# Optimization experiments

Hardware: AMD Instinct MI355X
Metric: run time of the kernel (lower is better)

Reference implementation:

```python
import jax, jax.numpy as jnp
import numpy as np

H = 4       # num_heads
K = 16      # neighbors
EPS = 1e-5  # BatchNorm eps (eval mode with running stats)


def _bn1d(y, g, b, m, v):
    # y: [B, C, N]; per-channel affine batchnorm (eval mode)
    return (y - m[:, None]) * (g[:, None] / jnp.sqrt(v[:, None] + EPS)) + b[:, None]


def setup_inputs() -> dict:
    key = jax.random.key(0)
    ks = jax.random.split(key, 10)
    B, C, N = 2, 256, 4096
    s = 0.02
    inp = {
        'x': jax.random.normal(ks[0], (B, C, N), jnp.float32),
        'xyz': jax.random.normal(ks[1], (B, 3, N), jnp.float32),
        'Wq': jax.random.normal(ks[2], (C, C), jnp.float32) * s,
        'Wkv': jax.random.normal(ks[3], (2 * C, C), jnp.float32) * s,
        'Wproj': jax.random.normal(ks[4], (C, C), jnp.float32) * s,
        'rp_w1': jax.random.normal(ks[5], (C, 3), jnp.float32) * s,
        'rp_g': jnp.ones((C,), jnp.float32),
        'rp_b': jnp.zeros((C,), jnp.float32),
        'rp_m': jnp.zeros((C,), jnp.float32),
        'rp_v': jnp.ones((C,), jnp.float32),
        'rp_w2': jax.random.normal(ks[6], (C, C), jnp.float32) * s,
        'bn1_g': jnp.ones((C,), jnp.float32), 'bn1_b': jnp.zeros((C,), jnp.float32),
        'bn1_m': jnp.zeros((C,), jnp.float32), 'bn1_v': jnp.ones((C,), jnp.float32),
        'bn2_g': jnp.ones((C,), jnp.float32), 'bn2_b': jnp.zeros((C,), jnp.float32),
        'bn2_m': jnp.zeros((C,), jnp.float32), 'bn2_v': jnp.ones((C,), jnp.float32),
        'ffn_w1': jax.random.normal(ks[7], (4 * C, C), jnp.float32) * s,
        'ffn_b1': jnp.zeros((4 * C,), jnp.float32),
        'ffn_w2': jax.random.normal(ks[8], (C, 4 * C), jnp.float32) * s,
        'ffn_b2': jnp.zeros((C,), jnp.float32),
    }
    return inp


def reference(x, xyz, Wq, Wkv, Wproj, rp_w1, rp_g, rp_b, rp_m, rp_v, rp_w2,
              bn1_g, bn1_b, bn1_m, bn1_v, bn2_g, bn2_b, bn2_m, bn2_v,
              ffn_w1, ffn_b1, ffn_w2, ffn_b2):
    B, C, N = x.shape
    d = C // H
    scale = d ** -0.5

    # --- KNN indices ---
    pts = xyz.transpose(0, 2, 1)                       # [B,N,3]
    sq = jnp.sum(pts * pts, -1)                        # [B,N]
    dists = sq[:, :, None] + sq[:, None, :] - 2.0 * jnp.einsum('bnc,bmc->bnm', pts, pts)
    idx = jax.lax.top_k(-dists, K)[1]                  # [B,N,K]

    # --- q, k, v (1x1 conv == matmul over channels) ---
    q = jnp.einsum('oc,bcn->bon', Wq, x).reshape(B, H, d, N)
    kv = jnp.einsum('oc,bcn->bon', Wkv, x)
    kf = kv[:, :C].transpose(0, 2, 1)                  # [B,N,C]
    vf = kv[:, C:].transpose(0, 2, 1)                  # [B,N,C]

    gather = jax.vmap(lambda f, i: f[i])               # per-batch KNN gather
    kg = gather(kf, idx).reshape(B, N, K, H, d)
    vg = gather(vf, idx).reshape(B, N, K, H, d)

    # --- attention logits: per-neighbor dot ---
    logits = jnp.einsum('bhdn,bnkhd->bhnk', q, kg) * scale

    # --- relative-position bias (1x1 conv MLP over rel coords) ---
    nbr = gather(pts, idx)                             # [B,N,K,3]
    rel = nbr - pts[:, :, None, :]                     # [B,N,K,3]
    h1 = jnp.einsum('oc,bnkc->bnko', rp_w1, rel)
    h1 = (h1 - rp_m) * (rp_g / jnp.sqrt(rp_v + EPS)) + rp_b
    h1 = jax.nn.relu(h1)
    h2 = jnp.einsum('oc,bnkc->bnko', rp_w2, h1).reshape(B, N, K, H, d)
    logits = logits + jnp.einsum('bnkhd->bhnk', h2)    # sum over d

    attn = jax.nn.softmax(logits, axis=-1)             # [B,H,N,K]
    out = jnp.einsum('bhnk,bnkhd->bhdn', attn, vg).reshape(B, C, N)
    out = jnp.einsum('oc,bcn->bon', Wproj, out)

    x1 = _bn1d(x + out, bn1_g, bn1_b, bn1_m, bn1_v)
    h = jax.nn.relu(jnp.einsum('oc,bcn->bon', ffn_w1, x1) + ffn_b1[:, None])
    f = jnp.einsum('oc,bcn->bon', ffn_w2, h) + ffn_b2[:, None]
    return _bn1d(x1 + f, bn2_g, bn2_b, bn2_m, bn2_v)
```

## Files before the change

### kernel.cpp

```cpp
#include <hip/hip_runtime.h>
#include <math.h>

#define BB   2
#define CC   256
#define NPT  4096
#define HH   4
#define DD   64
#define KNN  16
#define EPSBN 1e-5f

typedef __attribute__((ext_vector_type(8))) short short8;
typedef __attribute__((ext_vector_type(4))) float f32x4;

typedef __attribute__((address_space(3))) unsigned int lds_u32;
typedef const __attribute__((address_space(1))) unsigned int glb_u32;
__device__ __forceinline__ void gl_lds16(const void* g, void* l) {
  __builtin_amdgcn_global_load_lds((glb_u32*)g, (lds_u32*)l, 16, 0, 0);
}

__device__ __forceinline__ unsigned short f2b(float f) {
  union { float f; unsigned int u; } v; v.f = f;
  unsigned int r = (v.u + 0x7FFFu + ((v.u >> 16) & 1u)) >> 16;
  return (unsigned short)r;
}
__device__ __forceinline__ void up2(unsigned int u, float& a, float& b) {
  union { unsigned int x; float f; } lo, hi;
  lo.x = u << 16; hi.x = u & 0xffff0000u;
  a = lo.f; b = hi.f;
}
__device__ __forceinline__ void up16(uint4 u0, uint4 u1, float* f) {
  up2(u0.x, f[0], f[1]);  up2(u0.y, f[2], f[3]);
  up2(u0.z, f[4], f[5]);  up2(u0.w, f[6], f[7]);
  up2(u1.x, f[8], f[9]);  up2(u1.y, f[10], f[11]);
  up2(u1.z, f[12], f[13]); up2(u1.w, f[14], f[15]);
}

__device__ __forceinline__ unsigned int med3u(unsigned int a, unsigned int b, unsigned int c) {
  unsigned int d;
  asm("v_med3_u32 %0, %1, %2, %3" : "=v"(d) : "v"(a), "v"(b), "v"(c));
  return d;
}

__device__ __forceinline__
void wcast_body(const float* Wq, const float* Wkv, const float* Wp,
                const float* W1, const float* W2,
                unsigned short* oQKV, unsigned short* oP,
                unsigned short* o1, unsigned short* o2,
                const float* rp_w1, const float* rp_g, const float* rp_b,
                const float* rp_m, const float* rp_v, const float* rp_w2,
                float4* w1f, float4* W2t, int blk) {
  if (blk == 3072) {
    int c = threadIdx.x;
    float s  = rp_g[c] / sqrtf(rp_v[c] + EPSBN);
    float b0 = rp_b[c] - rp_m[c] * s;
    w1f[c] = make_float4(rp_w1[c*3+0]*s, rp_w1[c*3+1]*s, rp_w1[c*3+2]*s, b0);
    float a0=0.f,a1=0.f,a2=0.f,a3=0.f;
    for (int o = 0; o < 64; o++) {
      a0 += rp_w2[(      o)*CC + c];
      a1 += rp_w2[( 64 + o)*CC + c];
      a2 += rp_w2[(128 + o)*CC + c];
      a3 += rp_w2[(192 + o)*CC + c];
    }
    W2t[c] = make_float4(a0,a1,a2,a3);
    return;
  }
  int i = blk * 256 + threadIdx.x;
  if (i < 65536)        oQKV[i] = f2b(Wq[i]);
  else if (i < 196608)  oQKV[i] = f2b(Wkv[i - 65536]);
  else if (i < 262144)  oP[i - 196608] = f2b(Wp[i - 196608]);
  else if (i < 524288)  o1[i - 262144] = f2b(W1[i - 262144]);
  else                  o2[i - 524288] = f2b(W2[i - 524288]);
}

__device__ __forceinline__
void xcast_body(const float* x, unsigned short* xb, float* xf,
                float (*T)[65], int bx, int by, int bz) {
  int n0 = bx * 64, c0 = by * 64, bb = bz;
  int tid = threadIdx.x;
  {
    int crow = tid >> 2, ns = (tid & 3) * 16;
    const float* xp = x + ((size_t)(bb*CC + c0 + crow))*NPT + n0 + ns;
#pragma unroll
    for (int i = 0; i < 4; i++) {
      float4 v = ((const float4*)xp)[i];
      T[crow][ns + i*4 + 0] = v.x; T[crow][ns + i*4 + 1] = v.y;
      T[crow][ns + i*4 + 2] = v.z; T[crow][ns + i*4 + 3] = v.w;
    }
  }
  __syncthreads();
  {
    int nrow = tid >> 2, cs = (tid & 3) * 16;
    float vals[16];
#pragma unroll
    for (int i = 0; i < 16; i++) vals[i] = T[cs + i][nrow];
    size_t orow = ((size_t)(bb*NPT + n0 + nrow))*CC + c0 + cs;
#pragma unroll
    for (int i = 0; i < 4; i++)
      *(float4*)&xf[orow + i*4] = make_float4(vals[i*4], vals[i*4+1], vals[i*4+2], vals[i*4+3]);
    unsigned short us[16];
#pragma unroll
    for (int i = 0; i < 16; i++) us[i] = f2b(vals[i]);
    *(uint4*)&xb[orow]     = *(const uint4*)&us[0];
    *(uint4*)&xb[orow + 8] = *(const uint4*)&us[8];
  }
}

#define MPROC(M4, MI) { \
    float nd = fmaf(qx2, (M4).x, fmaf(qy2, (M4).y, fmaf(qz2, (M4).z, (M4).w + qsq))); \
    nd = fmaxf(nd, 0.f); \
    unsigned int key = (__float_as_uint(nd) & 0xFFFFFE00u) | (unsigned int)(MI); \
    k15 = med3u(key, k14, k15); k14 = med3u(key, k13, k14); \
    k13 = med3u(key, k12, k13); k12 = med3u(key, k11, k12); \
    k11 = med3u(key, k10, k11); k10 = med3u(key, k9,  k10); \
    k9  = med3u(key, k8,  k9 ); k8  = med3u(key, k7,  k8 ); \
    k7  = med3u(key, k6,  k7 ); k6  = med3u(key, k5,  k6 ); \
    k5  = med3u(key, k4,  k5 ); k4  = med3u(key, k3,  k4 ); \
    k3  = med3u(key, k2,  k3 ); k2  = med3u(key, k1,  k2 ); \
    k1  = med3u(key, k0,  k1 ); k0  = min(key, k0); }

__device__ __forceinline__
void knn_partial_body(const float* xyz, unsigned int* Pp, float4* sp,
                      int s, int qg, int b) {
  const float* base = xyz + (size_t)b * 3 * NPT;
  int c0 = s * 512;
  for (int i = threadIdx.x; i < 512; i += 256) {
    float mx = base[c0 + i], my = base[NPT + c0 + i], mz = base[2*NPT + c0 + i];
    sp[i] = make_float4(mx, my, mz, mx*mx + my*my + mz*mz);
  }
  int lane = threadIdx.x & 63;
  int wv   = threadIdx.x >> 6;
  int qn   = qg * 64 + lane;
  float qx = base[qn], qy = base[NPT + qn], qz = base[2*NPT + qn];
  float qsq = qx*qx + qy*qy + qz*qz;
  float qx2 = -2.f*qx, qy2 = -2.f*qy, qz2 = -2.f*qz;
  __syncthreads();

  unsigned int k0=0xFFFFFFFFu,k1=0xFFFFFFFFu,k2=0xFFFFFFFFu,k3=0xFFFFFFFFu,
               k4=0xFFFFFFFFu,k5=0xFFFFFFFFu,k6=0xFFFFFFFFu,k7=0xFFFFFFFFu,
               k8=0xFFFFFFFFu,k9=0xFFFFFFFFu,k10=0xFFFFFFFFu,k11=0xFFFFFFFFu,
               k12=0xFFFFFFFFu,k13=0xFFFFFFFFu,k14=0xFFFFFFFFu,k15=0xFFFFFFFFu;

  int sb = wv * 128;
  for (int mm = 0; mm < 128; mm += 4) {
    float4 a = sp[sb+mm], bq = sp[sb+mm+1], cq = sp[sb+mm+2], dq = sp[sb+mm+3];
    MPROC(a,  sb+mm)
    MPROC(bq, sb+mm+1)
    MPROC(cq, sb+mm+2)
    MPROC(dq, sb+mm+3)
  }

  int gq = b * NPT + qn;
  uint4* out = (uint4*)(Pp + (size_t)gq * 512 + (size_t)(s*4 + wv) * 16);
  out[0] = make_uint4(k0,  k1,  k2,  k3);
  out[1] = make_uint4(k4,  k5,  k6,  k7);
  out[2] = make_uint4(k8,  k9,  k10, k11);
  out[3] = make_uint4(k12, k13, k14, k15);
}

__global__ __launch_bounds__(256) __attribute__((amdgpu_waves_per_eu(1, 4)))
void stage1_kernel(const float* x, unsigned short* xb, float* xf,
                   const float* xyz, unsigned int* Pp,
                   const float* Wq, const float* Wkv, const float* Wp,
                   const float* W1, const float* W2,
                   unsigned short* oQKV, unsigned short* oP,
                   unsigned short* o1, unsigned short* o2,
                   const float* rp_w1, const float* rp_g, const float* rp_b,
                   const float* rp_m, const float* rp_v, const float* rp_w2,
                   float4* w1f, float4* W2t) {
  __shared__ __align__(16) char smem[64*65*4];
  int bi = blockIdx.x;
  if (bi < 1024) {
    knn_partial_body(xyz, Pp, (float4*)smem, bi & 7, (bi >> 3) & 63, bi >> 9);
  } else if (bi < 1536) {
    int i = bi - 1024;
    xcast_body(x, xb, xf, (float(*)[65])smem, i & 63, (i >> 6) & 3, i >> 8);
  } else {
    wcast_body(Wq, Wkv, Wp, W1, W2, oQKV, oP, o1, o2,
               rp_w1, rp_g, rp_b, rp_m, rp_v, rp_w2, w1f, W2t, bi - 1536);
  }
}

__device__ __forceinline__ unsigned long long min64(unsigned long long a, unsigned long long b) {
  return a < b ? a : b;
}
__device__ __forceinline__ void ce64(unsigned long long& x, unsigned long long& y) {
  unsigned long long a = x, b = y;
  bool lt = a < b;
  x = lt ? a : b;
  y = lt ? b : a;
}
__device__ __forceinline__
void knn_merge_body(const unsigned int* Pp, int* idx_out, int blk) {
  int wv   = threadIdx.x >> 6;
  int lane = threadIdx.x & 63;
  int gq   = blk * 4 + wv;
  const uint4* base = (const uint4*)(Pp + (size_t)gq * 512);
  uint4 v0 = base[lane*2], v1 = base[lane*2 + 1];
  unsigned int gb = (unsigned int)(lane >> 3) * 512u;
  unsigned long long a[16];
  {
    unsigned int ks[8] = {v0.x, v0.y, v0.z, v0.w, v1.x, v1.y, v1.z, v1.w};
#pragma unroll
    for (int t = 0; t < 8; t++)
      a[t] = ((unsigned long long)(ks[t] & 0xFFFFFE00u) << 32) | (gb + (ks[t] & 0x1FFu));
#pragma unroll
    for (int t = 8; t < 16; t++) a[t] = ~0ull;
  }
#pragma unroll
  for (int r = 0; r < 6; r++) {
    const int m = 1 << r;
    unsigned long long t[16];
#pragma unroll
    for (int i = 0; i < 16; i++) {
      unsigned long long pb = __shfl_xor(a[15 - i], m, 64);
      t[i] = min64(a[i], pb);
    }
    if (r < 5) {
#pragma unroll
      for (int d = 8; d >= 1; d >>= 1)
#pragma unroll
        for (int i = 0; i < 16; i++)
          if ((i & d) == 0) ce64(t[i], t[i + d]);
    }
#pragma unroll
    for (int i = 0; i < 16; i++) a[i] = t[i];
  }
  if (lane == 0) {
    int4* o = (int4*)(idx_out + gq*16);
    o[0] = make_int4((int)(unsigned)a[0],  (int)(unsigned)a[1],
                     (int)(unsigned)a[2],  (int)(unsigned)a[3]);
    o[1] = make_int4((int)(unsigned)a[4],  (int)(unsigned)a[5],
                     (int)(unsigned)a[6],  (int)(unsigned)a[7]);
    o[2] = make_int4((int)(unsigned)a[8],  (int)(unsigned)a[9],
                     (int)(unsigned)a[10], (int)(unsigned)a[11]);
    o[3] = make_int4((int)(unsigned)a[12], (int)(unsigned)a[13],
                     (int)(unsigned)a[14], (int)(unsigned)a[15]);
  }
}

struct MG {
  const unsigned short* A; const unsigned short* Wt; int K; int M;
  unsigned short* OutB; float* OutF;
  const float* bias; const float* resid;
  const float* bng; const float* bnb; const float* bnm; const float* bnv;
};

template<int EPI, int NT>
__device__ __forceinline__ void mgemm_body(const MG& p, int bx, int by, int bz) {
  __shared__ unsigned short As[NT*64*64];
  __shared__ unsigned short Bs[64*64];
  const int tid  = threadIdx.x;
  const int bb   = bz;
  const int n0   = bx * (NT*64);
  const int m0   = by * 64;
  const int lane = tid & 63;
  const int wv   = tid >> 6;
  const int l15  = lane & 15;
  const int quad = lane >> 4;
  const int K    = p.K;
  const int WR   = NT*16;

  f32x4 acc[NT][4];
#pragma unroll
  for (int i = 0; i < NT; i++)
#pragma unroll
    for (int j = 0; j < 4; j++) acc[i][j] = (f32x4){0.f, 0.f, 0.f, 0.f};

  const int srow = wv*8 + (lane >> 3);
  const int pseg = lane & 7;
  const unsigned short* Abase = p.A  + (size_t)bb*NPT*K;

  for (int c0 = 0; c0 < K; c0 += 64) {
#pragma unroll
    for (int t = 0; t < NT*2; t++) {
      int row = t*32 + srow;
      int ls  = pseg ^ (row & 7);
      gl_lds16(Abase + (size_t)(n0 + row)*K + c0 + ls*8,
               &As[wv*512 + t*2048 + lane*8]);
    }
#pragma unroll
    for (int t = 0; t < 2; t++) {
      int row = t*32 + srow;
      int ls  = pseg ^ (row & 7);
      gl_lds16(p.Wt + (size_t)(m0 + row)*K + c0 + ls*8,
               &Bs[wv*512 + t*2048 + lane*8]);
    }
    __syncthreads();
    short8 bf[4][2];
#pragma unroll
    for (int mt = 0; mt < 4; mt++)
#pragma unroll
      for (int kk = 0; kk < 2; kk++) {
        int row = mt*16 + l15;
        int ps  = (kk*4 + quad) ^ (row & 7);
        bf[mt][kk] = *(const short8*)&Bs[row*64 + ps*8];
      }
#pragma unroll
    for (int nt = 0; nt < NT; nt++)
#pragma unroll
      for (int kk = 0; kk < 2; kk++) {
        int row = wv*WR + nt*16 + l15;
        int ps  = (kk*4 + quad) ^ (row & 7);
        short8 af = *(const short8*)&As[row*64 + ps*8];
#pragma unroll
        for (int mt = 0; mt < 4; mt++)
          acc[nt][mt] = __builtin_amdgcn_mfma_f32_16x16x32_bf16(af, bf[mt][kk], acc[nt][mt], 0, 0, 0);
      }
    __syncthreads();
  }

  if (EPI == 0 || EPI == 1) {
    float bs[4];
#pragma unroll
    for (int mt = 0; mt < 4; mt++)
      bs[mt] = (EPI == 1) ? p.bias[m0 + mt*16 + l15] : 0.f;
#pragma unroll
    for (int nt = 0; nt < NT; nt++)
#pragma unroll
      for (int reg = 0; reg < 4; reg++) {
        size_t row = ((size_t)(bb*NPT + n0 + wv*WR + nt*16 + quad*4 + reg))*p.M + m0;
#pragma unroll
        for (int mt = 0; mt < 4; mt++) {
          float v = acc[nt][mt][reg] + bs[mt];
          if (EPI == 1) v = fmaxf(v, 0.f);
          p.OutB[row + mt*16 + l15] = f2b(v);
        }
      }
  } else if (EPI == 2) {
    float sc[4], sh[4];
#pragma unroll
    for (int mt = 0; mt < 4; mt++) {
      int m = m0 + mt*16 + l15;
      float s = p.bng[m] / sqrtf(p.bnv[m] + EPSBN);
      sc[mt] = s; sh[mt] = p.bnb[m] - p.bnm[m]*s;
    }
#pragma unroll
    for (int nt = 0; nt < NT; nt++)
#pragma unroll
      for (int reg = 0; reg < 4; reg++) {
        size_t row = ((size_t)(bb*NPT + n0 + wv*WR + nt*16 + quad*4 + reg))*p.M + m0;
#pragma unroll
        for (int mt = 0; mt < 4; mt++) {
          float r = p.resid[row + mt*16 + l15];
          float v = (acc[nt][mt][reg] + r)*sc[mt] + sh[mt];
          p.OutF[row + mt*16 + l15] = v;
          p.OutB[row + mt*16 + l15] = f2b(v);
        }
      }
  } else {
    __shared__ float Tb[4][4][16*17];
    float sc[4], sh[4], bs[4];
#pragma unroll
    for (int mt = 0; mt < 4; mt++) {
      int m = m0 + mt*16 + l15;
      float s = p.bng[m] / sqrtf(p.bnv[m] + EPSBN);
      sc[mt] = s; sh[mt] = p.bnb[m] - p.bnm[m]*s;
      bs[mt] = p.bias[m];
    }
#pragma unroll
    for (int nt = 0; nt < NT; nt++) {
#pragma unroll
      for (int reg = 0; reg < 4; reg++) {
        size_t row = ((size_t)(bb*NPT + n0 + wv*WR + nt*16 + quad*4 + reg))*p.M + m0;
#pragma unroll
        for (int mt = 0; mt < 4; mt++) {
          float r = p.resid[row + mt*16 + l15];
          float v = (acc[nt][mt][reg] + bs[mt] + r)*sc[mt] + sh[mt];
          Tb[wv][mt][(quad*4 + reg)*17 + l15] = v;
        }
      }
      __syncthreads();
#pragma unroll
      for (int mt = 0; mt < 4; mt++)
#pragma unroll
        for (int reg = 0; reg < 4; reg++) {
          float v = Tb[wv][mt][l15*17 + quad*4 + reg];
          p.OutF[((size_t)(bb*p.M + m0 + mt*16 + quad*4 + reg))*NPT
                 + n0 + wv*WR + nt*16 + l15] = v;
        }
      __syncthreads();
    }
  }
}

template<int EPI, int NT>
__global__ __launch_bounds__(256)
void mgemm_kernel(MG p) { mgemm_body<EPI, NT>(p, blockIdx.x, blockIdx.y, blockIdx.z); }

__global__ __launch_bounds__(256)
void stage2_kernel(const unsigned int* Pp, int* idx, MG pqkv) {
  int bi = blockIdx.x;
  if (bi < 2048) {
    knn_merge_body(Pp, idx, bi);
  } else {
    int i = bi - 2048;
    mgemm_body<0, 2>(pqkv, i & 31, (i >> 5) % 12, i / 384);
  }
}

__global__ __launch_bounds__(256, 4)
void attn_kernel(const unsigned short* __restrict__ qkv, const float4* __restrict__ w1f,
                 const float4* __restrict__ W2t, const float* __restrict__ xyz,
                 const int* __restrict__ idx, unsigned short* __restrict__ attn_b) {
  __shared__ float4 sw1[256];
  __shared__ float4 sw2[256];
  __shared__ int   sidx[4][16];
  __shared__ float srel[4][16][4];
  __shared__ float sbias[4][16][4];
  __shared__ float red[4][16*68];
  int tid = threadIdx.x;
  int bn0 = blockIdx.x * 4;
  int b   = bn0 >> 12;
  sw1[tid] = w1f[tid];
  sw2[tid] = W2t[tid];
  if (tid < 64) {
    int p = tid >> 4, kk = tid & 15;
    int bn = bn0 + p, n = bn & 4095;
    int j = idx[bn*16 + kk];
    sidx[p][kk] = j;
    const float* pb = xyz + (size_t)b * 3 * NPT;
    srel[p][kk][0] = pb[j]         - pb[n];
    srel[p][kk][1] = pb[NPT + j]   - pb[NPT + n];
    srel[p][kk][2] = pb[2*NPT + j] - pb[2*NPT + n];
  }
  __syncthreads();
  {
    int kk = tid >> 4, cs = tid & 15;
    float rx[4], ry[4], rz[4], h[4][4];
#pragma unroll
    for (int p = 0; p < 4; p++) {
      rx[p] = srel[p][kk][0]; ry[p] = srel[p][kk][1]; rz[p] = srel[p][kk][2];
#pragma unroll
      for (int q = 0; q < 4; q++) h[p][q] = 0.f;
    }
#pragma unroll
    for (int i = 0; i < 16; i++) {
      int c = cs*16 + ((i + cs) & 15);
      float4 w  = sw1[c];
      float4 w2 = sw2[c];
#pragma unroll
      for (int p = 0; p < 4; p++) {
        float t0 = fmaxf(fmaf(rx[p], w.x, fmaf(ry[p], w.y, fmaf(rz[p], w.z, w.w))), 0.f);
        h[p][0] = fmaf(t0, w2.x, h[p][0]); h[p][1] = fmaf(t0, w2.y, h[p][1]);
        h[p][2] = fmaf(t0, w2.z, h[p][2]); h[p][3] = fmaf(t0, w2.w, h[p][3]);
      }
    }
#pragma unroll
    for (int off = 1; off < 16; off <<= 1)
#pragma unroll
      for (int p = 0; p < 4; p++)
#pragma unroll
        for (int q = 0; q < 4; q++)
          h[p][q] += __shfl_xor(h[p][q], off, 64);
    if (cs == 0)
#pragma unroll
      for (int p = 0; p < 4; p++)
#pragma unroll
        for (int q = 0; q < 4; q++) sbias[p][kk][q] = h[p][q];
  }
  __syncthreads();
  int wv   = tid >> 6;
  int lane = tid & 63;
  int k    = lane >> 2;
  int c4   = lane & 3;
  int ch0  = wv*64 + c4*16;
  size_t base = (size_t)(b*NPT) * 768;
#pragma unroll 1
  for (int p = 0; p < 4; p++) {
    int bn = bn0 + p;
    size_t rowq = (size_t)bn * 768;
    float qf[16];
    {
      uint4 q0 = *(const uint4*)(qkv + rowq + ch0);
      uint4 q1 = *(const uint4*)(qkv + rowq + ch0 + 8);
      up16(q0, q1, qf);
    }
    int j = sidx[p][k];
    float dot = 0.f;
    {
      const unsigned short* krow = qkv + base + (size_t)j*768 + 256 + ch0;
      uint4 k0 = *(const uint4*)(krow);
      uint4 k1 = *(const uint4*)(krow + 8);
      float kf[16];
      up16(k0, k1, kf);
#pragma unroll
      for (int i = 0; i < 16; i++) dot = fmaf(qf[i], kf[i], dot);
    }
    dot += __shfl_xor(dot, 1, 64);
    dot += __shfl_xor(dot, 2, 64);
    float logit = dot * 0.125f + sbias[p][k][wv];
    float mx = logit;
#pragma unroll
    for (int off = 4; off < 64; off <<= 1) mx = fmaxf(mx, __shfl_xor(mx, off, 64));
    float e = __expf(logit - mx);
    float ssum = e;
#pragma unroll
    for (int off = 4; off < 64; off <<= 1) ssum += __shfl_xor(ssum, off, 64);
    float w = e / ssum;
    {
      const unsigned short* vrow = qkv + base + (size_t)j*768 + 512 + ch0;
      uint4 v0 = *(const uint4*)(vrow);
      uint4 v1 = *(const uint4*)(vrow + 8);
      float vf[16];
      up16(v0, v1, vf);
      float* dst = &red[wv][k*68 + c4*16];
#pragma unroll
      for (int g = 0; g < 4; g++)
        ((float4*)dst)[g] = make_float4(w*vf[g*4], w*vf[g*4+1], w*vf[g*4+2], w*vf[g*4+3]);
    }
    __syncthreads();
    float o = 0.f;
#pragma unroll
    for (int kk2 = 0; kk2 < 16; kk2++) o += red[wv][kk2*68 + lane];
    attn_b[(size_t)bn*256 + wv*64 + lane] = f2b(o);
    __syncthreads();
  }
}

extern "C" void kernel_launch(void* const* d_in, const int* in_sizes, int n_in,
                              void* d_out, int out_size, void* d_ws, size_t ws_size,
                              hipStream_t stream) {
  const float* x     = (const float*)d_in[0];
  const float* xyz   = (const float*)d_in[1];
  const float* Wq    = (const float*)d_in[2];
  const float* Wkv   = (const float*)d_in[3];
  const float* Wproj = (const float*)d_in[4];
  const float* rp_w1 = (const float*)d_in[5];
  const float* rp_g  = (const float*)d_in[6];
  const float* rp_b  = (const float*)d_in[7];
  const float* rp_m  = (const float*)d_in[8];
  const float* rp_v  = (const float*)d_in[9];
  const float* rp_w2 = (const float*)d_in[10];
  const float* bn1_g = (const float*)d_in[11];
  const float* bn1_b = (const float*)d_in[12];
  const float* bn1_m = (const float*)d_in[13];
  const float* bn1_v = (const float*)d_in[14];
  const float* bn2_g = (const float*)d_in[15];
  const float* bn2_b = (const float*)d_in[16];
  const float* bn2_m = (const float*)d_in[17];
  const float* bn2_v = (const float*)d_in[18];
  const float* ffn_w1 = (const float*)d_in[19];
  const float* ffn_b1 = (const float*)d_in[20];
  const float* ffn_w2 = (const float*)d_in[21];
  const float* ffn_b2 = (const float*)d_in[22];

  char* ws = (char*)d_ws;
  float4* w1f = (float4*)(ws + 0);
  float4* W2t = (float4*)(ws + 4096);
  int*    idx = (int*)  (ws + 8192);
  const size_t oA = 532480;
  unsigned int*   Pp     = (unsigned int*)(ws + oA);
  unsigned short* attn_b = (unsigned short*)(ws + oA);
  float*          x1f    = (float*)(ws + oA + (4u<<20));
  unsigned short* x1b    = (unsigned short*)(ws + oA + (12u<<20));
  unsigned short* h_b    = (unsigned short*)(ws + oA + (16u<<20));
  const size_t oB = oA + (32u<<20);
  unsigned short* Wqkv_b  = (unsigned short*)(ws + oB);
  unsigned short* Wproj_b = (unsigned short*)(ws + oB + 393216);
  unsigned short* W1_b    = (unsigned short*)(ws + oB + 524288);
  unsigned short* W2_b    = (unsigned short*)(ws + oB + 1048576);
  unsigned short* xb      = (unsigned short*)(ws + oB + 1572864);
  float*          xf      = (float*)(ws + oB + 1572864 + (4u<<20));
  unsigned short* qkv     = (unsigned short*)(ws + oB + 1572864 + (12u<<20));

  stage1_kernel<<<4609, 256, 0, stream>>>(x, xb, xf, xyz, Pp,
                                          Wq, Wkv, Wproj, ffn_w1, ffn_w2,
                                          Wqkv_b, Wproj_b, W1_b, W2_b,
                                          rp_w1, rp_g, rp_b, rp_m, rp_v, rp_w2,
                                          w1f, W2t);

  MG pqkv = {xb, Wqkv_b, 256, 768, qkv, nullptr,
             nullptr, nullptr, nullptr, nullptr, nullptr, nullptr};
  stage2_kernel<<<2816, 256, 0, stream>>>(Pp, idx, pqkv);

  attn_kernel<<<(BB*NPT)/4, 256, 0, stream>>>(qkv, w1f, W2t, xyz, idx, attn_b);

  MG pproj = {attn_b, Wproj_b, 256, 256, x1b, x1f,
              nullptr, xf, bn1_g, bn1_b, bn1_m, bn1_v};
  mgemm_kernel<2, 1><<<dim3(64, 4, BB), 256, 0, stream>>>(pproj);

  MG pf1 = {x1b, W1_b, 256, 1024, h_b, nullptr,
            ffn_b1, nullptr, nullptr, nullptr, nullptr, nullptr};
  mgemm_kernel<1, 2><<<dim3(32, 16, BB), 256, 0, stream>>>(pf1);

  MG pf2 = {h_b, W2_b, 1024, 256, nullptr, (float*)d_out,
            ffn_b2, x1f, bn2_g, bn2_b, bn2_m, bn2_v};
  mgemm_kernel<3, 1><<<dim3(64, 4, BB), 256, 0, stream>>>(pf2);
}
```

Measured before the change: 222.1 us.

## Merge KNN partial top-16 lists within block via LDS before global write

Each KNN partial block now merges its four per-wave top-16 lists through shared memory with bitonic merges, so only one list per 512-candidate chunk is written. The partial buffer shrinks fourfold, and the merge stage reads 8 lists per query with one query per 8 lanes, running 3 shuffle rounds instead of 6 on a much smaller grid. The GEMM blocks are scheduled first in stage2. This adds LDS traffic and barriers to the partial kernel and enlarges its shared memory, which may lower occupancy.

```diff
diff --git a/kernel.cpp b/kernel.cpp
--- a/kernel.cpp
+++ b/kernel.cpp
@@ -39,6 +39,10 @@
   unsigned int d;
   asm("v_med3_u32 %0, %1, %2, %3" : "=v"(d) : "v"(a), "v"(b), "v"(c));
   return d;
+}
+__device__ __forceinline__ void ce32(unsigned int& x, unsigned int& y) {
+  unsigned int a = min(x, y), b = max(x, y);
+  x = a; y = b;
 }
 
 __device__ __forceinline__
@@ -119,8 +123,9 @@
     k1  = med3u(key, k0,  k1 ); k0  = min(key, k0); }
 
 __device__ __forceinline__
-void knn_partial_body(const float* xyz, unsigned int* Pp, float4* sp,
+void knn_partial_body(const float* xyz, unsigned int* Pp, char* smem,
                       int s, int qg, int b) {
+  float4* sp = (float4*)smem;
   const float* base = xyz + (size_t)b * 3 * NPT;
   int c0 = s * 512;
   for (int i = threadIdx.x; i < 512; i += 256) {
@@ -142,19 +147,43 @@
 
   int sb = wv * 128;
   for (int mm = 0; mm < 128; mm += 4) {
-    float4 a = sp[sb+mm], bq = sp[sb+mm+1], cq = sp[sb+mm+2], dq = sp[sb+mm+3];
-    MPROC(a,  sb+mm)
+    float4 a4 = sp[sb+mm], bq = sp[sb+mm+1], cq = sp[sb+mm+2], dq = sp[sb+mm+3];
+    MPROC(a4, sb+mm)
     MPROC(bq, sb+mm+1)
     MPROC(cq, sb+mm+2)
     MPROC(dq, sb+mm+3)
   }
 
-  int gq = b * NPT + qn;
-  uint4* out = (uint4*)(Pp + (size_t)gq * 512 + (size_t)(s*4 + wv) * 16);
-  out[0] = make_uint4(k0,  k1,  k2,  k3);
-  out[1] = make_uint4(k4,  k5,  k6,  k7);
-  out[2] = make_uint4(k8,  k9,  k10, k11);
-  out[3] = make_uint4(k12, k13, k14, k15);
+  unsigned int a[16] = {k0,k1,k2,k3,k4,k5,k6,k7,k8,k9,k10,k11,k12,k13,k14,k15};
+  unsigned int* L = (unsigned int*)smem;
+  int me = (wv*64 + lane)*17;
+  __syncthreads();
+#pragma unroll
+  for (int pw = 1; pw <= 2; pw <<= 1) {
+#pragma unroll
+    for (int i = 0; i < 16; i++) L[me + i] = a[i];
+    __syncthreads();
+    int pb = ((wv ^ pw)*64 + lane)*17;
+    unsigned int t[16];
+#pragma unroll
+    for (int i = 0; i < 16; i++) t[i] = min(a[i], L[pb + 15 - i]);
+#pragma unroll
+    for (int d = 8; d >= 1; d >>= 1)
+#pragma unroll
+      for (int i = 0; i < 16; i++)
+        if ((i & d) == 0) ce32(t[i], t[i + d]);
+#pragma unroll
+    for (int i = 0; i < 16; i++) a[i] = t[i];
+    __syncthreads();
+  }
+  if (wv == 0) {
+    int gq = b * NPT + qn;
+    uint4* out = (uint4*)(Pp + (size_t)gq * 128 + s * 16);
+    out[0] = make_uint4(a[0],  a[1],  a[2],  a[3]);
+    out[1] = make_uint4(a[4],  a[5],  a[6],  a[7]);
+    out[2] = make_uint4(a[8],  a[9],  a[10], a[11]);
+    out[3] = make_uint4(a[12], a[13], a[14], a[15]);
+  }
 }
 
 __global__ __launch_bounds__(256) __attribute__((amdgpu_waves_per_eu(1, 4)))
@@ -167,10 +196,10 @@
                    const float* rp_w1, const float* rp_g, const float* rp_b,
                    const float* rp_m, const float* rp_v, const float* rp_w2,
                    float4* w1f, float4* W2t) {
-  __shared__ __align__(16) char smem[64*65*4];
+  __shared__ __align__(16) char smem[17408];
   int bi = blockIdx.x;
   if (bi < 1024) {
-    knn_partial_body(xyz, Pp, (float4*)smem, bi & 7, (bi >> 3) & 63, bi >> 9);
+    knn_partial_body(xyz, Pp, smem, bi & 7, (bi >> 3) & 63, bi >> 9);
   } else if (bi < 1536) {
     int i = bi - 1024;
     xcast_body(x, xb, xf, (float(*)[65])smem, i & 63, (i >> 6) & 3, i >> 8);
@@ -193,21 +222,21 @@
 void knn_merge_body(const unsigned int* Pp, int* idx_out, int blk) {
   int wv   = threadIdx.x >> 6;
   int lane = threadIdx.x & 63;
-  int gq   = blk * 4 + wv;
-  const uint4* base = (const uint4*)(Pp + (size_t)gq * 512);
-  uint4 v0 = base[lane*2], v1 = base[lane*2 + 1];
-  unsigned int gb = (unsigned int)(lane >> 3) * 512u;
+  int gq   = (blk*4 + wv)*8 + (lane >> 3);
+  int s    = lane & 7;
+  const uint4* src = (const uint4*)(Pp + (size_t)gq * 128 + s * 16);
+  uint4 u0 = src[0], u1 = src[1], u2 = src[2], u3 = src[3];
+  unsigned int gb = (unsigned int)s * 512u;
   unsigned long long a[16];
   {
-    unsigned int ks[8] = {v0.x, v0.y, v0.z, v0.w, v1.x, v1.y, v1.z, v1.w};
-#pragma unroll
-    for (int t = 0; t < 8; t++)
+    unsigned int ks[16] = {u0.x,u0.y,u0.z,u0.w, u1.x,u1.y,u1.z,u1.w,
+                           u2.x,u2.y,u2.z,u2.w, u3.x,u3.y,u3.z,u3.w};
+#pragma unroll
+    for (int t = 0; t < 16; t++)
       a[t] = ((unsigned long long)(ks[t] & 0xFFFFFE00u) << 32) | (gb + (ks[t] & 0x1FFu));
-#pragma unroll
-    for (int t = 8; t < 16; t++) a[t] = ~0ull;
-  }
-#pragma unroll
-  for (int r = 0; r < 6; r++) {
+  }
+#pragma unroll
+  for (int r = 0; r < 3; r++) {
     const int m = 1 << r;
     unsigned long long t[16];
 #pragma unroll
@@ -215,7 +244,7 @@
       unsigned long long pb = __shfl_xor(a[15 - i], m, 64);
       t[i] = min64(a[i], pb);
     }
-    if (r < 5) {
+    if (r < 2) {
 #pragma unroll
       for (int d = 8; d >= 1; d >>= 1)
 #pragma unroll
@@ -225,7 +254,7 @@
 #pragma unroll
     for (int i = 0; i < 16; i++) a[i] = t[i];
   }
-  if (lane == 0) {
+  if (s == 0) {
     int4* o = (int4*)(idx_out + gq*16);
     o[0] = make_int4((int)(unsigned)a[0],  (int)(unsigned)a[1],
                      (int)(unsigned)a[2],  (int)(unsigned)a[3]);
@@ -390,11 +419,10 @@
 __global__ __launch_bounds__(256)
 void stage2_kernel(const unsigned int* Pp, int* idx, MG pqkv) {
   int bi = blockIdx.x;
-  if (bi < 2048) {
-    knn_merge_body(Pp, idx, bi);
+  if (bi < 768) {
+    mgemm_body<0, 2>(pqkv, bi & 31, (bi >> 5) % 12, bi / 384);
   } else {
-    int i = bi - 2048;
-    mgemm_body<0, 2>(pqkv, i & 31, (i >> 5) % 12, i / 384);
+    knn_merge_body(Pp, idx, bi - 768);
   }
 }
 
@@ -571,7 +599,7 @@
 
   MG pqkv = {xb, Wqkv_b, 256, 768, qkv, nullptr,
              nullptr, nullptr, nullptr, nullptr, nullptr, nullptr};
-  stage2_kernel<<<2816, 256, 0, stream>>>(Pp, idx, pqkv);
+  stage2_kernel<<<1024, 256, 0, stream>>>(Pp, idx, pqkv);
 
   attn_kernel<<<(BB*NPT)/4, 256, 0, stream>>>(qkv, w1f, W2t, xyz, idx, attn_b);
 
```

Result: faster. 194.8 us (-12.3%).
